# Kernel tuning notes

Measured on AMD Instinct MI355X. Metric: run time of the kernel, lower is better.

Reference implementation:

```python
import jax, jax.numpy as jnp
import numpy as np

RPN_CLS_NEGATIVE = -1
RPN_CLS_NEUTRAL = 0
RPN_CLS_POSITIVE = 1

A = 261888  # anchors for 1024x1024 FPN, 3 per location
G = 256     # gt boxes


def _make_boxes(key, n, max_tl=900.0, min_sz=16.0, max_sz=124.0):
    k1, k2 = jax.random.split(key)
    tl = jax.random.uniform(k1, (n, 2), dtype=jnp.float32) * max_tl  # (y1, x1)
    wh = min_sz + jax.random.uniform(k2, (n, 2), dtype=jnp.float32) * (max_sz - min_sz)
    return jnp.concatenate([tl, tl + wh], axis=1)  # (y1, x1, y2, x2), all coords > 0


def setup_inputs() -> dict:
    key = jax.random.key(0)
    ka, kg, km, kc = jax.random.split(key, 4)
    anchors = _make_boxes(ka, A)
    gt_boxes = _make_boxes(kg, G)
    valid_anchors_mask = jax.random.uniform(km, (A,)) > 0.1
    gt_class_ids = jax.random.randint(kc, (G,), 1, 81, dtype=jnp.int32)
    bbox_std_dev = jnp.array([0.1, 0.1, 0.2, 0.2], dtype=jnp.float32)
    return {
        "anchors": anchors,
        "valid_anchors_mask": valid_anchors_mask,
        "gt_class_ids": gt_class_ids,
        "gt_boxes": gt_boxes,
        "bbox_std_dev": bbox_std_dev,
    }


def _compute_overlaps(b1, b2):
    """Pairwise IoU. b1: [N,4], b2: [M,4] -> [N,M]."""
    y1 = jnp.maximum(b1[:, None, 0], b2[None, :, 0])
    x1 = jnp.maximum(b1[:, None, 1], b2[None, :, 1])
    y2 = jnp.minimum(b1[:, None, 2], b2[None, :, 2])
    x2 = jnp.minimum(b1[:, None, 3], b2[None, :, 3])
    inter = jnp.maximum(y2 - y1, 0.0) * jnp.maximum(x2 - x1, 0.0)
    area1 = (b1[:, 2] - b1[:, 0]) * (b1[:, 3] - b1[:, 1])
    area2 = (b2[:, 2] - b2[:, 0]) * (b2[:, 3] - b2[:, 1])
    union = area1[:, None] + area2[None, :] - inter
    return inter / union


def reference(anchors, valid_anchors_mask, gt_class_ids, gt_boxes, bbox_std_dev):
    num_anchors = anchors.shape[0]
    is_crowd = gt_class_ids < 0  # [G]
    any_crowd = jnp.any(is_crowd)

    overlaps = _compute_overlaps(anchors, gt_boxes)  # [A, G]

    # crowd suppression (vectorized equivalent of the numpy crowd branch)
    crowd_iou_max = jnp.max(jnp.where(is_crowd[None, :], overlaps, 0.0), axis=1)
    no_crowd = jnp.where(any_crowd, crowd_iou_max < 0.001, True)

    # mask crowd columns out of the matching (numpy filters them from gt_boxes)
    ov = jnp.where(is_crowd[None, :], -1.0, overlaps)  # [A, G]
    anchor_iou_argmax = jnp.argmax(ov, axis=1)          # [A]
    anchor_iou_max = jnp.max(ov, axis=1)                # [A]

    # per-GT best anchor, restricted to valid anchors (numpy works on valid subset)
    ov_valid = jnp.where(valid_anchors_mask[:, None], ov, -1.0)
    gt_iou_argmax = jnp.argmax(ov_valid, axis=0)        # [G]
    pos_from_gt = jnp.zeros((num_anchors,), dtype=bool).at[gt_iou_argmax].max(~is_crowd)

    positive = pos_from_gt | (anchor_iou_max >= 0.7)
    negative = (anchor_iou_max < 0.3) & no_crowd & (~positive)

    rpn_match = jnp.where(positive, RPN_CLS_POSITIVE,
                          jnp.where(negative, RPN_CLS_NEGATIVE, RPN_CLS_NEUTRAL)).astype(jnp.int32)
    rpn_match = jnp.where(valid_anchors_mask, rpn_match, RPN_CLS_NEUTRAL)

    # deltas for positive anchors (faithful to source, incl. the `- -` -> `+` size bug)
    matched_gt = gt_boxes[anchor_iou_argmax]            # [A, 4]
    gt_size = matched_gt[:, 2:4] + matched_gt[:, 0:2]   # source: b[:,2:4] - -b[:,0:2]
    gt_centre = (matched_gt[:, 0:2] + matched_gt[:, 2:4]) * 0.5
    anc_size = anchors[:, 2:4] + anchors[:, 0:2]        # same bug
    anc_centre = (anchors[:, 0:2] + anchors[:, 2:4]) * 0.5
    deltas = jnp.concatenate([(gt_centre - anc_centre) / anc_size,
                              jnp.log(gt_size / anc_size)], axis=1)  # [A, 4]
    deltas = deltas / bbox_std_dev[None, :]  # RPN_BBOX_USE_STD_DEV = True

    pos_valid = positive & valid_anchors_mask
    rpn_bbox_all = jnp.where(pos_valid[:, None], deltas, 0.0).astype(jnp.float32)
    num_positives = jnp.sum(pos_valid).astype(jnp.int32)
    return rpn_match, rpn_bbox_all, num_positives
```

## Files before the change

kernel.cpp:

```cpp
#include <hip/hip_runtime.h>


#define GMAX 256
#define SHARDS 16
#define KBIAS 0xC0000001u
#define AIMASK 0x3FFFFu

__device__ __forceinline__ float4 compute_deltas(float4 ab, float4 gb,
                                                 const float* __restrict__ sd) {
    float sy_g = gb.z + gb.x;
    float sx_g = gb.w + gb.y;
    float sy_a = ab.z + ab.x;
    float sx_a = ab.w + ab.y;
    float4 d;
    d.x = (0.5f * (sy_g - sy_a) / sy_a) / sd[0];
    d.y = (0.5f * (sx_g - sx_a) / sx_a) / sd[1];
    d.z = logf(sy_g / sy_a) / sd[2];
    d.w = logf(sx_g / sx_a) / sd[3];
    return d;
}

__device__ __forceinline__ float iou_from(float4 ab, float a_area, float4 gb,
                                          float ga, float& inter) {
#pragma clang fp contract(off)
    float y1 = fmaxf(ab.x, gb.x);
    float x1 = fmaxf(ab.y, gb.y);
    float y2 = fminf(ab.z, gb.z);
    float x2 = fminf(ab.w, gb.w);
    inter = fmaxf(y2 - y1, 0.f) * fmaxf(x2 - x1, 0.f);
    return inter * __builtin_amdgcn_rcpf((a_area + ga) - inter);
}

__device__ __forceinline__ float iou_of(float4 ab, float a_area, float4 gb) {
    float y1 = fmaxf(ab.x, gb.x);
    float x1 = fmaxf(ab.y, gb.y);
    float y2 = fminf(ab.z, gb.z);
    float x2 = fminf(ab.w, gb.w);
    float inter = fmaxf(y2 - y1, 0.f) * fmaxf(x2 - x1, 0.f);
    float garea = (gb.z - gb.x) * (gb.w - gb.y);
    float uni = (a_area + garea) - inter;
    return inter * __builtin_amdgcn_rcpf(uni);
}

__device__ __forceinline__ float sel4f(float a0, float a1, float a2, float a3, int h) {
    float lo = (h & 1) ? a1 : a0;
    float hi = (h & 1) ? a3 : a2;
    return (h & 2) ? hi : lo;
}
__device__ __forceinline__ int sel4i(int a0, int a1, int a2, int a3, int h) {
    int lo = (h & 1) ? a1 : a0;
    int hi = (h & 1) ? a3 : a2;
    return (h & 2) ? hi : lo;
}
__device__ __forceinline__ float4 sel4f4(float4 a0, float4 a1, float4 a2, float4 a3, int h) {
    float4 r;
    r.x = sel4f(a0.x, a1.x, a2.x, a3.x, h);
    r.y = sel4f(a0.y, a1.y, a2.y, a3.y, h);
    r.z = sel4f(a0.z, a1.z, a2.z, a3.z, h);
    r.w = sel4f(a0.w, a1.w, a2.w, a3.w, h);
    return r;
}

__global__ __launch_bounds__(256, 4) void rpn_main11(
    const float4* __restrict__ anchors,
    const int* __restrict__ valid,
    const int* __restrict__ cls,
    const float4* __restrict__ gt,
    const float* __restrict__ stdev,
    float* __restrict__ out,
    unsigned long long* __restrict__ gkeyS,
    int* __restrict__ pcount,
    int* __restrict__ fvmin,
    int A, int G)
{
    __shared__ float4 s_gt[GMAX];
    __shared__ float s_area[GMAX];
    __shared__ float s_crowdf[GMAX];
    __shared__ unsigned long long s_key[GMAX];
    __shared__ int s_anycrowd, s_cnt, s_fv;

    const int tid = threadIdx.x;
    if (tid == 0) { s_anycrowd = 0; s_cnt = 0; s_fv = 0x7FFFFFFF; }
    s_key[tid] = 0ULL;
    if (tid < G) {
        float4 b = gt[tid];
        s_gt[tid] = b;
        s_area[tid] = (b.z - b.x) * (b.w - b.y);
        int c = cls[tid];
        s_crowdf[tid] = (c < 0) ? 1.0f : 0.0f;
        if (c < 0) s_anycrowd = 1;
    }
    __syncthreads();
    const int any_crowd = s_anycrowd;

    const int q = tid >> 2;
    const int h = tid & 3;
    const int abase = blockIdx.x * 256 + (q << 2);
    const int myai  = blockIdx.x * 256 + tid;
    const bool myir = (myai < A);

    bool posv = false, vmy = false;

    if (!any_crowd && G == GMAX) {
        float4 ab[4]; float aar[4]; int vld[4];
        #pragma unroll
        for (int k = 0; k < 4; ++k) {
            const int ak = abase + k;
            const bool irk = (ak < A);
            ab[k]  = irk ? anchors[ak] : make_float4(0.f, 0.f, 1.f, 1.f);
            vld[k] = irk ? valid[ak] : 0;
            aar[k] = (ab[k].z - ab[k].x) * (ab[k].w - ab[k].y);
        }

        unsigned mlo[4] = {0u, 0u, 0u, 0u};
        unsigned mhi[4] = {0u, 0u, 0u, 0u};
        const float4* gp = &s_gt[h];
        #pragma unroll 8
        for (int j = 0; j < 32; ++j) {
            float4 gb = gp[j << 2];
            const unsigned bit = 1u << j;
            #pragma unroll
            for (int k = 0; k < 4; ++k) {
                bool ovy = (ab[k].x < gb.z) && (gb.x < ab[k].z);
                bool ovx = (ab[k].y < gb.w) && (gb.y < ab[k].w);
                mlo[k] |= (ovy && ovx) ? bit : 0u;
            }
        }
        #pragma unroll 8
        for (int j = 0; j < 32; ++j) {
            float4 gb = gp[(j + 32) << 2];
            const unsigned bit = 1u << j;
            #pragma unroll
            for (int k = 0; k < 4; ++k) {
                bool ovy = (ab[k].x < gb.z) && (gb.x < ab[k].z);
                bool ovx = (ab[k].y < gb.w) && (gb.y < ab[k].w);
                mhi[k] |= (ovy && ovx) ? bit : 0u;
            }
        }

        float mb4[4]; int bg4[4];
        #pragma unroll
        for (int k = 0; k < 4; ++k) {
            float bb = 0.f; int bg = 0x7FFFFFFF;
            unsigned long long m = ((unsigned long long)mhi[k] << 32) | mlo[k];
            while (m != 0ULL) {
                int j = __builtin_ctzll(m); m &= (m - 1ULL);
                int g = (j << 2) + h;
                float it;
                float iou = iou_from(ab[k], aar[k], s_gt[g], s_area[g], it);
                if (iou > bb) { bb = iou; bg = g; }
            }
            #pragma unroll
            for (int off = 1; off <= 2; off <<= 1) {
                float ob = __shfl_xor(bb, off);
                int  obg = __shfl_xor(bg, off);
                if (ob > bb || (ob == bb && obg < bg)) { bb = ob; bg = obg; }
            }
            mb4[k] = bb;
            bg4[k] = (bg == 0x7FFFFFFF) ? 0 : bg;
        }

        const float4 abm  = sel4f4(ab[0], ab[1], ab[2], ab[3], h);
        const float  mbm  = sel4f(mb4[0], mb4[1], mb4[2], mb4[3], h);
        const int    bgmy = sel4i(bg4[0], bg4[1], bg4[2], bg4[3], h);
        const int    vm   = sel4i(vld[0], vld[1], vld[2], vld[3], h);
        vmy = myir && (vm != 0);
        bool pos = (mbm >= 0.7f);
        bool neg = (mbm < 0.3f) && !pos;
        posv = pos && vmy;
        if (myir) {
            out[myai] = vmy ? (pos ? 1.0f : (neg ? -1.0f : 0.0f)) : 0.0f;
            float4 d = make_float4(0.f, 0.f, 0.f, 0.f);
            if (pos && vmy) d = compute_deltas(abm, s_gt[bgmy], stdev);
            ((float4*)(out + A))[myai] = d;
        }

        #pragma unroll
        for (int k = 0; k < 4; ++k) {
            if (vld[k]) {
                const unsigned long long lo =
                    (((unsigned long long)((~(unsigned)(abase + k)) & AIMASK)) << 8) |
                    (unsigned long long)((unsigned)bg4[k] & 0xFFu);
                unsigned long long m = ((unsigned long long)mhi[k] << 32) | mlo[k];
                while (m != 0ULL) {
                    int j = __builtin_ctzll(m); m &= (m - 1ULL);
                    int g = (j << 2) + h;
                    float it;
                    float iou = iou_from(ab[k], aar[k], s_gt[g], s_area[g], it);
                    atomicMax(&s_key[g],
                        (((unsigned long long)(__float_as_uint(iou) + KBIAS)) << 32) | lo);
                }
            }
        }
    } else {
        float4 ab2 = myir ? anchors[myai] : make_float4(0.f, 0.f, 1.f, 1.f);
        int v2 = myir ? valid[myai] : 0;
        float aa2 = (ab2.z - ab2.x) * (ab2.w - ab2.y);
        float bb = -2.f; int bg = 0; float cmx = 0.f;
        unsigned long long mk[4] = {0ULL, 0ULL, 0ULL, 0ULL};
        #pragma unroll
        for (int w = 0; w < 4; ++w) {
            unsigned long long m = 0ULL;
            for (int j = 0; j < 64; ++j) {
                int g = (w << 6) + j;
                if (g >= G) break;
                float it;
                float iou = iou_from(ab2, aa2, s_gt[g], s_area[g], it);
                float cf = s_crowdf[g];
                float eff = (cf != 0.f) ? -1.f : iou;
                if (eff > bb) { bb = eff; bg = g; }
                cmx = fmaxf(cmx, iou * cf);
                if (cf == 0.f && it > 0.f) m |= (1ULL << j);
            }
            mk[w] = m;
        }
        bool no_crowd = (cmx < 0.001f);
        vmy = myir && (v2 != 0);
        bool pos = (bb >= 0.7f);
        bool neg = (bb < 0.3f) && no_crowd && !pos;
        posv = pos && vmy;
        if (myir) {
            out[myai] = vmy ? (pos ? 1.0f : (neg ? -1.0f : 0.0f)) : 0.0f;
            float4 d = make_float4(0.f, 0.f, 0.f, 0.f);
            if (pos && vmy) d = compute_deltas(ab2, s_gt[bg], stdev);
            ((float4*)(out + A))[myai] = d;
        }
        if (vmy) {
            const unsigned long long lo =
                (((unsigned long long)((~(unsigned)myai) & AIMASK)) << 8) |
                (unsigned long long)((unsigned)bg & 0xFFu);
            #pragma unroll
            for (int w = 0; w < 4; ++w) {
                unsigned long long m = mk[w];
                while (m != 0ULL) {
                    int j = __builtin_ctzll(m); m &= (m - 1ULL);
                    int g = (w << 6) + j;
                    float it;
                    float iou = iou_from(ab2, aa2, s_gt[g], s_area[g], it);
                    atomicMax(&s_key[g],
                        (((unsigned long long)(__float_as_uint(iou) + KBIAS)) << 32) | lo);
                }
            }
        }
    }

    unsigned long long bal = __ballot((int)posv);
    if ((tid & 63) == 0) atomicAdd(&s_cnt, (int)__popcll(bal));
    unsigned long long vb = __ballot((int)vmy);
    if ((tid & 63) == 0 && vb != 0ULL)
        atomicMin(&s_fv, (int)(blockIdx.x * 256 + (tid & ~63) + (int)__builtin_ctzll(vb)));
    __syncthreads();

    if (tid < G && s_key[tid] != 0ULL)
        atomicMax(&gkeyS[(size_t)tid * SHARDS + (blockIdx.x & (SHARDS - 1))],
                  s_key[tid]);
    if (tid == 0) { pcount[blockIdx.x] = s_cnt; fvmin[blockIdx.x] = s_fv; }
}

__global__ __launch_bounds__(1024) void rpn_finalize4(
    const float4* __restrict__ anchors,
    const int* __restrict__ cls,
    const float4* __restrict__ gt,
    const float* __restrict__ stdev,
    float* __restrict__ out,
    const unsigned long long* __restrict__ gkeyS,
    const int* __restrict__ pcount,
    const int* __restrict__ fvmin,
    int nb, int A, int G)
{
    __shared__ float4 s_gt[GMAX];
    __shared__ float s_area[GMAX];
    __shared__ float s_crowdf[GMAX];
    __shared__ int s_tot, s_fvr, s_flip;

    const int tid = threadIdx.x;
    if (tid == 0) { s_tot = 0; s_fvr = 0x7FFFFFFF; s_flip = 0; }
    if (tid < G) {
        float4 b = gt[tid];
        s_gt[tid] = b;
        s_area[tid] = (b.z - b.x) * (b.w - b.y);
        s_crowdf[tid] = (cls[tid] < 0) ? 1.0f : 0.0f;
    }
    __syncthreads();

    unsigned long long key = 0ULL;
    if (tid < G) {
        const unsigned long long* p = gkeyS + (size_t)tid * SHARDS;
        #pragma unroll
        for (int s = 0; s < SHARDS; s += 2) {
            ulonglong2 kv = *reinterpret_cast<const ulonglong2*>(p + s);
            unsigned long long k = (kv.x > kv.y) ? kv.x : kv.y;
            key = (k > key) ? k : key;
        }
    }
    if (tid >= 256) {
        int acc = 0, fv = 0x7FFFFFFF;
        for (int i = tid - 256; i < nb; i += 768) {
            acc += pcount[i];
            fv = min(fv, fvmin[i]);
        }
        #pragma unroll
        for (int off = 32; off >= 1; off >>= 1) {
            acc += __shfl_xor(acc, off);
            fv = min(fv, __shfl_xor(fv, off));
        }
        if ((tid & 63) == 0) { atomicAdd(&s_tot, acc); atomicMin(&s_fvr, fv); }
    }
    __syncthreads();

    bool flipped = false;
    if (tid < G && s_crowdf[tid] == 0.0f) {
        const bool has = ((unsigned)(key >> 32) >= (KBIAS + 1u));
        int w = -1, bg = -1;
        if (has) {
            w  = (int)((~((unsigned)key >> 8)) & AIMASK);
            bg = (int)((unsigned)key & 0xFFu);
        } else if (s_fvr != 0x7FFFFFFF) {
            w = s_fvr;
        }
        if (w >= 0) {
            float old = atomicExch(out + w, 1.0f);
            if (old != 1.0f) {
                if (bg < 0) {
                    float4 ab = anchors[w];
                    float aa = (ab.z - ab.x) * (ab.w - ab.y);
                    float bb = -2.0f; bg = 0;
                    for (int g = 0; g < G; ++g) {
                        float it;
                        float iou = iou_from(ab, aa, s_gt[g], s_area[g], it);
                        float eff = (s_crowdf[g] != 0.0f) ? -1.0f : iou;
                        if (eff > bb) { bb = eff; bg = g; }
                    }
                }
                ((float4*)(out + A))[w] = compute_deltas(anchors[w], s_gt[bg], stdev);
                flipped = true;
            }
        }
    }
    unsigned long long fb = __ballot((int)flipped);
    if (tid < 256 && (tid & 63) == 0) atomicAdd(&s_flip, (int)__popcll(fb));
    __syncthreads();
    if (tid == 0) out[(size_t)5 * A] = (float)(s_tot + s_flip);
}

__global__ __launch_bounds__(256) void rpn_fused(
    const float4* __restrict__ anchors, const int* __restrict__ valid,
    const int* __restrict__ cls, const float4* __restrict__ gt,
    const float* __restrict__ stdev, float* __restrict__ out,
    unsigned long long* __restrict__ gkey, unsigned* __restrict__ done,
    int* __restrict__ cnt, int A, int G)
{
    __shared__ float4 s_gt[GMAX];
    __shared__ float s_crowdf[GMAX];
    __shared__ unsigned long long s_key[GMAX];
    __shared__ int s_anycrowd; __shared__ int s_cnt; __shared__ int s_islast;

    const int tid = threadIdx.x;
    if (tid == 0) { s_anycrowd = 0; s_cnt = 0; }
    if (tid < G) {
        s_gt[tid] = gt[tid];
        int c = cls[tid];
        s_crowdf[tid] = (c < 0) ? 1.0f : 0.0f;
        if (c < 0) s_anycrowd = 1;
        s_key[tid] = 0ULL;
    }
    __syncthreads();
    const int any_crowd = s_anycrowd;
    const int ai = blockIdx.x * 256 + tid;
    const bool in_range = (ai < A);
    float4 ab = in_range ? anchors[ai] : make_float4(0.f, 0.f, 1.f, 1.f);
    const bool v = in_range && (valid[ai] != 0);
    const float a_area = (ab.z - ab.x) * (ab.w - ab.y);
    const unsigned lokey = ~(unsigned)ai;

    float best = any_crowd ? -2.0f : -1.0f;
    int bg = 0; float crowd_max = 0.0f;
    unsigned long long ovmask[4];
    #pragma unroll
    for (int w = 0; w < 4; ++w) {
        unsigned long long m = 0ULL;
        #pragma unroll 4
        for (int j = 0; j < 64; ++j) {
            int g = (w << 6) + j;
            if (g >= G) break;
            float iou = iou_of(ab, a_area, s_gt[g]);
            float cf = s_crowdf[g];
            float eff = (any_crowd && cf != 0.0f) ? -1.0f : iou;
            if (eff > best) { best = eff; bg = g; }
            if (any_crowd) crowd_max = fmaxf(crowd_max, iou * cf);
            if (v && (cf == 0.0f) && iou > 0.0f) m |= (1ULL << j);
        }
        ovmask[w] = m;
    }
    #pragma unroll
    for (int w = 0; w < 4; ++w) {
        unsigned long long m = ovmask[w];
        while (m != 0ULL) {
            int j = __builtin_ctzll(m); m &= (m - 1ULL);
            int g = (w << 6) + j;
            float iou = iou_of(ab, a_area, s_gt[g]);
            atomicMax(&s_key[g],
                (((unsigned long long)(__float_as_uint(iou) + 1u)) << 32) | lokey);
        }
    }
    bool no_crowd = any_crowd ? (crowd_max < 0.001f) : true;
    bool pos = (best >= 0.7f);
    bool neg = (best < 0.3f) && no_crowd && !pos;
    unsigned long long pv = __ballot((int)(in_range && pos && v));
    if ((tid & 63) == 0) atomicAdd(&s_cnt, (int)__popcll(pv));
    if (in_range) {
        out[ai] = v ? (pos ? 1.0f : (neg ? -1.0f : 0.0f)) : 0.0f;
        float4 d = make_float4(0.f, 0.f, 0.f, 0.f);
        if (pos && v) d = compute_deltas(ab, s_gt[bg], stdev);
        ((float4*)(out + A))[ai] = d;
    }
    __syncthreads();
    if (tid < G && s_key[tid] != 0ULL) atomicMax(&gkey[tid], s_key[tid]);
    if (tid == 0 && s_cnt > 0) atomicAdd(cnt, s_cnt);
    __threadfence();
    if (tid == 0) {
        unsigned prev = atomicAdd(done, 1u);
        s_islast = (prev == gridDim.x - 1);
        s_cnt = 0;
    }
    __syncthreads();
    if (!s_islast) return;
    __threadfence();
    if (tid < G && s_crowdf[tid] == 0.0f) {
        unsigned long long key = gkey[tid];
        int w;
        if (key != 0ULL) w = (int)(~(unsigned)(key & 0xFFFFFFFFull));
        else { w = 0; for (int i = 0; i < A; ++i) { if (valid[i] != 0) { w = i; break; } } }
        if (valid[w] != 0) {
            float old = atomicExch(out + w, 1.0f);
            if (old != 1.0f) {
                float4 ab2 = anchors[w];
                float a2 = (ab2.z - ab2.x) * (ab2.w - ab2.y);
                float b2 = -2.0f; int g2 = 0;
                for (int g = 0; g < G; ++g) {
                    float iou = iou_of(ab2, a2, s_gt[g]);
                    float eff = (s_crowdf[g] != 0.0f) ? -1.0f : iou;
                    if (eff > b2) { b2 = eff; g2 = g; }
                }
                ((float4*)(out + A))[w] = compute_deltas(ab2, s_gt[g2], stdev);
                atomicAdd(&s_cnt, 1);
            }
        }
    }
    __syncthreads();
    if (tid == 0) out[(size_t)5 * A] = (float)(*cnt + s_cnt);
}

extern "C" void kernel_launch(void* const* d_in, const int* in_sizes, int n_in,
                              void* d_out, int out_size, void* d_ws, size_t ws_size,
                              hipStream_t stream) {
    const float4* anchors = (const float4*)d_in[0];
    const int* valid      = (const int*)d_in[1];
    const int* cls        = (const int*)d_in[2];
    const float4* gtb     = (const float4*)d_in[3];
    const float* stdev    = (const float*)d_in[4];
    float* out            = (float*)d_out;

    const int A = in_sizes[0] / 4;
    const int G = in_sizes[2];
    const int nb4 = (A + 255) / 256;

    const size_t shard_bytes = (size_t)G * SHARDS * 8;
    const size_t pcnt_bytes  = (size_t)nb4 * 4;
    const size_t fv_bytes    = (size_t)nb4 * 4;
    const size_t needed = shard_bytes + pcnt_bytes + fv_bytes;

    if (ws_size >= needed && G <= GMAX && A <= (1 << 18)) {
        char* p = (char*)d_ws;
        unsigned long long* gkeyS = (unsigned long long*)p;          p += shard_bytes;
        int* pcount               = (int*)p;                         p += pcnt_bytes;
        int* fvmin                = (int*)p;

        rpn_main11<<<nb4, 256, 0, stream>>>(anchors, valid, cls, gtb, stdev, out,
                                            gkeyS, pcount, fvmin, A, G);
        rpn_finalize4<<<1, 1024, 0, stream>>>(anchors, cls, gtb, stdev, out,
                                              gkeyS, pcount, fvmin, nb4, A, G);
    } else {
        const int nb = (A + 255) / 256;
        unsigned long long* gkey = (unsigned long long*)d_ws;
        unsigned* done = (unsigned*)((char*)d_ws + 2048);
        int* cnt       = (int*)((char*)d_ws + 2052);
        hipMemsetAsync(d_ws, 0, 2056, stream);
        rpn_fused<<<nb, 256, 0, stream>>>(anchors, valid, cls, gtb, stdev, out,
                                          gkey, done, cnt, A, G);
    }
}
```

Measured before the change: 100.9 us.

## Fuse per-GT atomicMax into argmax loop and store per-anchor argmax to workspace

Moves the shared-memory atomicMax for per-GT best anchor into the first overlap loop, so IoU is no longer computed a second time. Invalid anchors are replaced with far-away sentinel boxes so they never overlap and need no branch. The key now packs the full anchor index, and the per-anchor best GT is written to a workspace array that finalize reads, replacing its fallback IoU scan. The cost is an extra A-sized global write and atomics issued inside the argmax loop.

Measured after the change: 97.41 us (median of 2 runs). 1.04x faster.

```diff
diff --git a/kernel.cpp b/kernel.cpp
--- a/kernel.cpp
+++ b/kernel.cpp
@@ -4,7 +4,6 @@
 #define GMAX 256
 #define SHARDS 16
 #define KBIAS 0xC0000001u
-#define AIMASK 0x3FFFFu
 
 __device__ __forceinline__ float4 compute_deltas(float4 ab, float4 gb,
                                                  const float* __restrict__ sd) {
@@ -61,7 +60,7 @@
     return r;
 }
 
-__global__ __launch_bounds__(256, 4) void rpn_main11(
+__global__ __launch_bounds__(256, 4) void rpn_main12(
     const float4* __restrict__ anchors,
     const int* __restrict__ valid,
     const int* __restrict__ cls,
@@ -69,6 +68,7 @@
     const float* __restrict__ stdev,
     float* __restrict__ out,
     unsigned long long* __restrict__ gkeyS,
+    int* __restrict__ akey,
     int* __restrict__ pcount,
     int* __restrict__ fvmin,
     int A, int G)
@@ -107,9 +107,11 @@
         for (int k = 0; k < 4; ++k) {
             const int ak = abase + k;
             const bool irk = (ak < A);
-            ab[k]  = irk ? anchors[ak] : make_float4(0.f, 0.f, 1.f, 1.f);
+            float4 b = irk ? anchors[ak] : make_float4(0.f, 0.f, 1.f, 1.f);
             vld[k] = irk ? valid[ak] : 0;
-            aar[k] = (ab[k].z - ab[k].x) * (ab[k].w - ab[k].y);
+            if (!vld[k]) b = make_float4(3.0e30f, 3.0e30f, 3.0e30f, 3.0e30f);
+            ab[k]  = b;
+            aar[k] = (b.z - b.x) * (b.w - b.y);
         }
 
         unsigned mlo[4] = {0u, 0u, 0u, 0u};
@@ -142,6 +144,7 @@
         #pragma unroll
         for (int k = 0; k < 4; ++k) {
             float bb = 0.f; int bg = 0x7FFFFFFF;
+            const unsigned lokey = ~(unsigned)(abase + k);
             unsigned long long m = ((unsigned long long)mhi[k] << 32) | mlo[k];
             while (m != 0ULL) {
                 int j = __builtin_ctzll(m); m &= (m - 1ULL);
@@ -149,6 +152,8 @@
                 float it;
                 float iou = iou_from(ab[k], aar[k], s_gt[g], s_area[g], it);
                 if (iou > bb) { bb = iou; bg = g; }
+                atomicMax(&s_key[g],
+                    (((unsigned long long)(__float_as_uint(iou) + KBIAS)) << 32) | lokey);
             }
             #pragma unroll
             for (int off = 1; off <= 2; off <<= 1) {
@@ -173,24 +178,7 @@
             float4 d = make_float4(0.f, 0.f, 0.f, 0.f);
             if (pos && vmy) d = compute_deltas(abm, s_gt[bgmy], stdev);
             ((float4*)(out + A))[myai] = d;
-        }
-
-        #pragma unroll
-        for (int k = 0; k < 4; ++k) {
-            if (vld[k]) {
-                const unsigned long long lo =
-                    (((unsigned long long)((~(unsigned)(abase + k)) & AIMASK)) << 8) |
-                    (unsigned long long)((unsigned)bg4[k] & 0xFFu);
-                unsigned long long m = ((unsigned long long)mhi[k] << 32) | mlo[k];
-                while (m != 0ULL) {
-                    int j = __builtin_ctzll(m); m &= (m - 1ULL);
-                    int g = (j << 2) + h;
-                    float it;
-                    float iou = iou_from(ab[k], aar[k], s_gt[g], s_area[g], it);
-                    atomicMax(&s_key[g],
-                        (((unsigned long long)(__float_as_uint(iou) + KBIAS)) << 32) | lo);
-                }
-            }
+            akey[myai] = bgmy;
         }
     } else {
         float4 ab2 = myir ? anchors[myai] : make_float4(0.f, 0.f, 1.f, 1.f);
@@ -224,11 +212,10 @@
             float4 d = make_float4(0.f, 0.f, 0.f, 0.f);
             if (pos && vmy) d = compute_deltas(ab2, s_gt[bg], stdev);
             ((float4*)(out + A))[myai] = d;
+            akey[myai] = bg;
         }
         if (vmy) {
-            const unsigned long long lo =
-                (((unsigned long long)((~(unsigned)myai) & AIMASK)) << 8) |
-                (unsigned long long)((unsigned)bg & 0xFFu);
+            const unsigned lokey = ~(unsigned)myai;
             #pragma unroll
             for (int w = 0; w < 4; ++w) {
                 unsigned long long m = mk[w];
@@ -238,7 +225,7 @@
                     float it;
                     float iou = iou_from(ab2, aa2, s_gt[g], s_area[g], it);
                     atomicMax(&s_key[g],
-                        (((unsigned long long)(__float_as_uint(iou) + KBIAS)) << 32) | lo);
+                        (((unsigned long long)(__float_as_uint(iou) + KBIAS)) << 32) | lokey);
                 }
             }
         }
@@ -257,28 +244,26 @@
     if (tid == 0) { pcount[blockIdx.x] = s_cnt; fvmin[blockIdx.x] = s_fv; }
 }
 
-__global__ __launch_bounds__(1024) void rpn_finalize4(
+__global__ __launch_bounds__(1024) void rpn_finalize5(
     const float4* __restrict__ anchors,
     const int* __restrict__ cls,
     const float4* __restrict__ gt,
     const float* __restrict__ stdev,
     float* __restrict__ out,
     const unsigned long long* __restrict__ gkeyS,
+    const int* __restrict__ akey,
     const int* __restrict__ pcount,
     const int* __restrict__ fvmin,
     int nb, int A, int G)
 {
     __shared__ float4 s_gt[GMAX];
-    __shared__ float s_area[GMAX];
     __shared__ float s_crowdf[GMAX];
     __shared__ int s_tot, s_fvr, s_flip;
 
     const int tid = threadIdx.x;
     if (tid == 0) { s_tot = 0; s_fvr = 0x7FFFFFFF; s_flip = 0; }
     if (tid < G) {
-        float4 b = gt[tid];
-        s_gt[tid] = b;
-        s_area[tid] = (b.z - b.x) * (b.w - b.y);
+        s_gt[tid] = gt[tid];
         s_crowdf[tid] = (cls[tid] < 0) ? 1.0f : 0.0f;
     }
     __syncthreads();
@@ -311,27 +296,16 @@
     bool flipped = false;
     if (tid < G && s_crowdf[tid] == 0.0f) {
         const bool has = ((unsigned)(key >> 32) >= (KBIAS + 1u));
-        int w = -1, bg = -1;
+        int w = -1;
         if (has) {
-            w  = (int)((~((unsigned)key >> 8)) & AIMASK);
-            bg = (int)((unsigned)key & 0xFFu);
+            w = (int)(~(unsigned)(key & 0xFFFFFFFFull));
         } else if (s_fvr != 0x7FFFFFFF) {
             w = s_fvr;
         }
         if (w >= 0) {
             float old = atomicExch(out + w, 1.0f);
             if (old != 1.0f) {
-                if (bg < 0) {
-                    float4 ab = anchors[w];
-                    float aa = (ab.z - ab.x) * (ab.w - ab.y);
-                    float bb = -2.0f; bg = 0;
-                    for (int g = 0; g < G; ++g) {
-                        float it;
-                        float iou = iou_from(ab, aa, s_gt[g], s_area[g], it);
-                        float eff = (s_crowdf[g] != 0.0f) ? -1.0f : iou;
-                        if (eff > bb) { bb = eff; bg = g; }
-                    }
-                }
+                int bg = akey[w];
                 ((float4*)(out + A))[w] = compute_deltas(anchors[w], s_gt[bg], stdev);
                 flipped = true;
             }
@@ -466,20 +440,22 @@
     const int nb4 = (A + 255) / 256;
 
     const size_t shard_bytes = (size_t)G * SHARDS * 8;
+    const size_t akey_bytes  = (size_t)A * 4;
     const size_t pcnt_bytes  = (size_t)nb4 * 4;
     const size_t fv_bytes    = (size_t)nb4 * 4;
-    const size_t needed = shard_bytes + pcnt_bytes + fv_bytes;
-
-    if (ws_size >= needed && G <= GMAX && A <= (1 << 18)) {
+    const size_t needed = shard_bytes + akey_bytes + pcnt_bytes + fv_bytes;
+
+    if (ws_size >= needed && G <= GMAX) {
         char* p = (char*)d_ws;
         unsigned long long* gkeyS = (unsigned long long*)p;          p += shard_bytes;
+        int* akey                 = (int*)p;                         p += akey_bytes;
         int* pcount               = (int*)p;                         p += pcnt_bytes;
         int* fvmin                = (int*)p;
 
-        rpn_main11<<<nb4, 256, 0, stream>>>(anchors, valid, cls, gtb, stdev, out,
-                                            gkeyS, pcount, fvmin, A, G);
-        rpn_finalize4<<<1, 1024, 0, stream>>>(anchors, cls, gtb, stdev, out,
-                                              gkeyS, pcount, fvmin, nb4, A, G);
+        rpn_main12<<<nb4, 256, 0, stream>>>(anchors, valid, cls, gtb, stdev, out,
+                                            gkeyS, akey, pcount, fvmin, A, G);
+        rpn_finalize5<<<1, 1024, 0, stream>>>(anchors, cls, gtb, stdev, out,
+                                              gkeyS, akey, pcount, fvmin, nb4, A, G);
     } else {
         const int nb = (A + 255) / 256;
         unsigned long long* gkey = (unsigned long long*)d_ws;
```
